# Performance work log

Measured on AMD Instinct MI355X. Metric: run time of the kernel, lower is better.

Reference implementation:

```python
import jax, jax.numpy as jnp
import numpy as np

DIM = 1024
DIM_HEAD = 64
HEADS = 8
INNER = DIM_HEAD * HEADS
EPS = 1e-5


def layernorm(x, g, b):
    mu = jnp.mean(x, axis=-1, keepdims=True)
    var = jnp.var(x, axis=-1, keepdims=True)
    return (x - mu) * jax.lax.rsqrt(var + EPS) * g + b


def setup_inputs() -> dict:
    key = jax.random.key(0)
    ks = jax.random.split(key, 8)
    b, n, m = 8, 4096, 64
    x = jax.random.normal(ks[0], (b, n, DIM), dtype=jnp.float32)
    latents = jax.random.normal(ks[1], (b, m, DIM), dtype=jnp.float32)
    mask = jax.random.bernoulli(ks[2], 0.9, (b, n))
    s = DIM ** -0.5
    Wq = jax.random.normal(ks[3], (DIM, INNER), dtype=jnp.float32) * s
    Wkv = jax.random.normal(ks[4], (DIM, 2 * INNER), dtype=jnp.float32) * s
    Wo = jax.random.normal(ks[5], (INNER, DIM), dtype=jnp.float32) * (INNER ** -0.5)
    ln_x_g = jnp.ones((DIM,), jnp.float32); ln_x_b = jnp.zeros((DIM,), jnp.float32)
    ln_l_g = jnp.ones((DIM,), jnp.float32); ln_l_b = jnp.zeros((DIM,), jnp.float32)
    ln_o_g = jnp.ones((DIM,), jnp.float32); ln_o_b = jnp.zeros((DIM,), jnp.float32)
    return {"x": x, "latents": latents, "mask": mask,
            "Wq": Wq, "Wkv": Wkv, "Wo": Wo,
            "ln_x_g": ln_x_g, "ln_x_b": ln_x_b,
            "ln_l_g": ln_l_g, "ln_l_b": ln_l_b,
            "ln_o_g": ln_o_g, "ln_o_b": ln_o_b}


def reference(x, latents, mask, Wq, Wkv, Wo, ln_x_g, ln_x_b, ln_l_g, ln_l_b, ln_o_g, ln_o_b):
    scale = DIM_HEAD ** -0.5
    b, m = latents.shape[0], latents.shape[1]
    xn = layernorm(x, ln_x_g, ln_x_b)
    ln = layernorm(latents, ln_l_g, ln_l_b)
    q = ln @ Wq                                   # [b, m, inner]
    kv_in = jnp.concatenate([xn, ln], axis=1)     # [b, n+m, dim]
    kv = kv_in @ Wkv                              # [b, n+m, 2*inner]
    k, v = jnp.split(kv, 2, axis=-1)
    # b n (h d) -> b h n d
    q = q.reshape(b, m, HEADS, DIM_HEAD).transpose(0, 2, 1, 3)
    k = k.reshape(b, k.shape[1], HEADS, DIM_HEAD).transpose(0, 2, 1, 3)
    v = v.reshape(b, v.shape[1], HEADS, DIM_HEAD).transpose(0, 2, 1, 3)
    # NOTE: scale applied twice, faithful to the original module.
    sim = jnp.einsum('bhid,bhjd->bhij', q * scale, k) * scale
    full_mask = jnp.concatenate([mask, jnp.ones((b, m), dtype=bool)], axis=1)  # pad True for latents
    max_neg = -jnp.finfo(sim.dtype).max
    sim = jnp.where(full_mask[:, None, None, :], sim, max_neg)
    attn = jax.nn.softmax(sim.astype(jnp.float32), axis=-1).astype(sim.dtype)
    out = jnp.einsum('bhij,bhjd->bhid', attn, v)
    out = out.transpose(0, 2, 1, 3).reshape(b, m, INNER)
    out = out @ Wo
    return layernorm(out, ln_o_g, ln_o_b)
```

## Files before the change

kernel.cpp:

```cpp
#include <hip/hip_runtime.h>

typedef unsigned short u16;
typedef unsigned int u32;
using f32x4  = __attribute__((ext_vector_type(4))) float;
using short8 = __attribute__((ext_vector_type(8))) short;
using s16x4  = __attribute__((ext_vector_type(4))) short;
using u16x4  = __attribute__((ext_vector_type(4))) unsigned short;

#define DEV __device__ __forceinline__

DEV u16 f2bf(float f) {
  u32 u = __float_as_uint(f);
  u32 r = u + 0x7fffu + ((u >> 16) & 1u);
  return (u16)(r >> 16);
}

DEV void gload_lds16(const void* g, void* l) {
  __builtin_amdgcn_global_load_lds(
      (__attribute__((address_space(1))) void*)g,
      (__attribute__((address_space(3))) void*)l, 16, 0, 0);
}

DEV void block_reduce2(float& a, float& b, float* red) {
#pragma unroll
  for (int m = 1; m < 64; m <<= 1) {
    a += __shfl_xor(a, m);
    b += __shfl_xor(b, m);
  }
  const int wid = threadIdx.x >> 6, lane = threadIdx.x & 63;
  __syncthreads();
  if (lane == 0) { red[wid] = a; red[4 + wid] = b; }
  __syncthreads();
  a = red[0] + red[1] + red[2] + red[3];
  b = red[4] + red[5] + red[6] + red[7];
}

__global__ __launch_bounds__(256) void ln_rows_k(
    const float* __restrict__ X, const float* __restrict__ g,
    const float* __restrict__ be, u16* __restrict__ out, int mode)
{
  __shared__ float red[8];
  const int r = blockIdx.x, t = threadIdx.x;
  const float4 v = *(const float4*)(X + (((size_t)r) << 10) + t * 4);
  float s1 = v.x + v.y + v.z + v.w;
  float s2 = v.x * v.x + v.y * v.y + v.z * v.z + v.w * v.w;
  block_reduce2(s1, s2, red);
  const float mean = s1 * (1.f / 1024.f);
  const float var  = s2 * (1.f / 1024.f) - mean * mean;
  const float rstd = rsqrtf(var + 1e-5f);
  const float4 gv = *(const float4*)(g + t * 4);
  const float4 bv = *(const float4*)(be + t * 4);
  u16x4 o;
  o[0] = f2bf((v.x - mean) * rstd * gv.x + bv.x);
  o[1] = f2bf((v.y - mean) * rstd * gv.y + bv.y);
  o[2] = f2bf((v.z - mean) * rstd * gv.z + bv.z);
  o[3] = f2bf((v.w - mean) * rstd * gv.w + bv.w);
  const size_t orow = (mode == 0)
      ? ((size_t)(r >> 12) * 4160 + (r & 4095))
      : ((size_t)(r >> 6) * 4160 + 4096 + (r & 63));
  *(u16x4*)(out + orow * 1024 + t * 4) = o;
}

__global__ __launch_bounds__(256) void transpose_w_k(
    const float* __restrict__ W, u16* __restrict__ Wt, int K, int N)
{
  __shared__ float tile[32][33];
  const int n0 = blockIdx.x * 32, k0 = blockIdx.y * 32;
  const int tx = threadIdx.x, ty = threadIdx.y;
#pragma unroll
  for (int i = 0; i < 4; ++i)
    tile[ty + 8 * i][tx] = W[(size_t)(k0 + ty + 8 * i) * N + n0 + tx];
  __syncthreads();
#pragma unroll
  for (int i = 0; i < 4; ++i)
    Wt[(size_t)(n0 + ty + 8 * i) * K + k0 + tx] = f2bf(tile[tx][ty + 8 * i]);
}

__global__ __launch_bounds__(256) void mask_bias_k(const void* __restrict__ mask,
                                                   float* __restrict__ bias)
{
  __shared__ int flag_s;
  if (threadIdx.x == 0) {
    const u32* mw = (const u32*)mask;
    bool fpat = true, ipat = true;
    for (int i = 0; i < 256; ++i) {
      u32 w = mw[i];
      if (w != 0u && w != 0x3f800000u) fpat = false;
      if (w > 1u) ipat = false;
    }
    flag_s = fpat ? 2 : (ipat ? 1 : 0);
  }
  __syncthreads();
  const int flag = flag_s;
  const int idx = blockIdx.x * 256 + threadIdx.x;
  const int b = idx / 4160, j = idx - b * 4160;
  float bv = 0.f;
  if (j < 4096) {
    const int mi = b * 4096 + j;
    bool on;
    if (flag == 2)      on = ((const float*)mask)[mi] != 0.f;
    else if (flag == 1) on = ((const int*)mask)[mi] != 0;
    else                on = ((const unsigned char*)mask)[mi] != 0;
    bv = on ? 0.f : -1e30f;
  }
  bias[idx] = bv;
}

template <int MODE>
__global__ __launch_bounds__(256) void gemm_k(
    const u16* __restrict__ A, const u16* __restrict__ Bt, u16* __restrict__ out)
{
  __shared__ __attribute__((aligned(16))) short As[4096];
  __shared__ __attribute__((aligned(16))) short Bs[4096];
  const int tid = threadIdx.x;
  const int wid = tid >> 6, lane = tid & 63;
  const int wm = wid >> 1, wn = wid & 1;
  const int m0 = blockIdx.x * 128, n0 = blockIdx.y * 128;
  const f32x4 z4 = {0.f, 0.f, 0.f, 0.f};
  f32x4 acc[4][4];
#pragma unroll
  for (int i = 0; i < 4; ++i)
#pragma unroll
    for (int j = 0; j < 4; ++j) acc[i][j] = z4;

  for (int kt = 0; kt < 32; ++kt) {
    const int k0 = kt * 32;
#pragma unroll
    for (int p = 0; p < 2; ++p) {
      const int idx = p * 256 + tid;
      const int row = idx >> 2, seg = idx & 3;
      size_t ar;
      if (MODE == 1) {
        const int gr = m0 + row;
        ar = (size_t)(gr >> 6) * 4160 + 4096 + (gr & 63);
      } else {
        ar = (size_t)(m0 + row);
      }
      gload_lds16(A + ar * 1024 + k0 + seg * 8, &As[(p * 256 + wid * 64) * 8]);
    }
#pragma unroll
    for (int p = 0; p < 2; ++p) {
      const int idx = p * 256 + tid;
      const int row = idx >> 2, seg = idx & 3;
      gload_lds16(Bt + (size_t)(n0 + row) * 1024 + k0 + seg * 8,
                  &Bs[(p * 256 + wid * 64) * 8]);
    }
    __syncthreads();
    short8 af[4], bfr[4];
#pragma unroll
    for (int mi = 0; mi < 4; ++mi)
      af[mi] = *(const short8*)&As[(wm * 64 + mi * 16 + (lane & 15)) * 32 + 8 * (lane >> 4)];
#pragma unroll
    for (int ni = 0; ni < 4; ++ni)
      bfr[ni] = *(const short8*)&Bs[(wn * 64 + ni * 16 + (lane & 15)) * 32 + 8 * (lane >> 4)];
#pragma unroll
    for (int mi = 0; mi < 4; ++mi)
#pragma unroll
      for (int ni = 0; ni < 4; ++ni)
        acc[mi][ni] = __builtin_amdgcn_mfma_f32_16x16x32_bf16(af[mi], bfr[ni], acc[mi][ni], 0, 0, 0);
    __syncthreads();
  }

#pragma unroll
  for (int mi = 0; mi < 4; ++mi)
#pragma unroll
    for (int ni = 0; ni < 4; ++ni)
#pragma unroll
      for (int r = 0; r < 4; ++r) {
        const int gm = m0 + wm * 64 + mi * 16 + (lane >> 4) * 4 + r;
        const int gn = n0 + wn * 64 + ni * 16 + (lane & 15);
        const u16 v = f2bf(acc[mi][ni][r]);
        if (MODE == 0) {
          const int b = gm / 4160, j = gm - b * 4160;
          out[(((size_t)b * 8 + (gn >> 6)) * 4160 + j) * 64 + (gn & 63)] = v;
        } else if (MODE == 1) {
          const int b = gm >> 6, i = gm & 63;
          out[(((size_t)b * 8 + (gn >> 6)) * 64 + i) * 64 + (gn & 63)] = v;
        } else {
          const int b = gn / 4160, j = gn - b * 4160;
          out[(((size_t)b * 8 + (gm >> 6)) * 64 + (gm & 63)) * 4160 + j] = v;
        }
      }
}

__global__ __launch_bounds__(256) void attn_k(
    const u16* __restrict__ q_h, const u16* __restrict__ k_h,
    const u16* __restrict__ v_t, const float* __restrict__ bias,
    float* __restrict__ O_part, float* __restrict__ m_part,
    float* __restrict__ l_part)
{
  __shared__ __attribute__((aligned(16))) short Ks[4096];
  __shared__ __attribute__((aligned(16))) short Vs[4096];
  __shared__ __attribute__((aligned(16))) short Ps[4][1152];
  __shared__ float biasS[64];
  const int bid = blockIdx.x;
  const int sp = bid & 7, bh = bid >> 3;
  const int b = bh >> 3;
  const int tid = threadIdx.x, wid = tid >> 6, lane = tid & 63;
  const int t0 = sp ? (8 * sp + 1) : 0;
  const int tc = sp ? 8 : 9;

  const size_t qoff = ((size_t)bh * 64 + wid * 16 + (lane & 15)) * 64 + 8 * (lane >> 4);
  const short8 qf0 = *(const short8*)&q_h[qoff];
  const short8 qf1 = *(const short8*)&q_h[qoff + 32];

  float mrun = -1e30f, lrun = 0.f;
  const f32x4 z4 = {0.f, 0.f, 0.f, 0.f};
  f32x4 o[4] = {z4, z4, z4, z4};
  const size_t khead = (size_t)bh * (4160 * 64);
  const size_t vhead = (size_t)bh * (64 * 4160);

  for (int tt = 0; tt < tc; ++tt) {
    const int t = t0 + tt;
#pragma unroll
    for (int p = 0; p < 2; ++p) {
      const int lo = (p * 256 + tid) * 16;
      const int row = lo >> 7;
      const int src = lo ^ ((row & 7) << 4);
      gload_lds16((const char*)k_h + (khead + (size_t)t * 4096) * 2 + src,
                  (char*)Ks + (p * 256 + wid * 64) * 16);
    }
#pragma unroll
    for (int p = 0; p < 2; ++p) {
      const int lo = (p * 256 + tid) * 16;
      const int row = lo >> 7;
      const int colb = (lo ^ ((row & 7) << 4)) & 127;
      gload_lds16((const char*)v_t + (vhead + (size_t)row * 4160 + t * 64) * 2 + colb,
                  (char*)Vs + (p * 256 + wid * 64) * 16);
    }
    if (tid < 64) biasS[tid] = bias[b * 4160 + t * 64 + tid];
    __syncthreads();

    f32x4 sc[4] = {z4, z4, z4, z4};
#pragma unroll
    for (int mi = 0; mi < 4; ++mi) {
      const int row = mi * 16 + (lane & 15);
      const int sw = (row & 7) << 4;
      short8 a0 = *(const short8*)((const char*)Ks + ((row * 128 + 16 * (lane >> 4)) ^ sw));
      sc[mi] = __builtin_amdgcn_mfma_f32_16x16x32_bf16(a0, qf0, sc[mi], 0, 0, 0);
      short8 a1 = *(const short8*)((const char*)Ks + ((row * 128 + 64 + 16 * (lane >> 4)) ^ sw));
      sc[mi] = __builtin_amdgcn_mfma_f32_16x16x32_bf16(a1, qf1, sc[mi], 0, 0, 0);
    }

    float sv[4][4];
    float tmax = -3e30f;
#pragma unroll
    for (int mi = 0; mi < 4; ++mi)
#pragma unroll
      for (int r = 0; r < 4; ++r) {
        const int kv = mi * 16 + (lane >> 4) * 4 + r;
        const float s = sc[mi][r] * (1.f / 64.f) + biasS[kv];
        sv[mi][r] = s;
        tmax = fmaxf(tmax, s);
      }
    tmax = fmaxf(tmax, __shfl_xor(tmax, 16));
    tmax = fmaxf(tmax, __shfl_xor(tmax, 32));
    const float mnew = fmaxf(mrun, tmax);
    const float fac = __expf(mrun - mnew);
    float psum = 0.f;
#pragma unroll
    for (int mi = 0; mi < 4; ++mi) {
      s16x4 pk;
#pragma unroll
      for (int r = 0; r < 4; ++r) {
        const float p = __expf(sv[mi][r] - mnew);
        psum += p;
        pk[r] = (short)f2bf(p);
      }
      *(s16x4*)&Ps[wid][(lane & 15) * 72 + mi * 16 + (lane >> 4) * 4] = pk;
    }
    psum += __shfl_xor(psum, 16);
    psum += __shfl_xor(psum, 32);
    lrun = lrun * fac + psum;
    mrun = mnew;
#pragma unroll
    for (int mi = 0; mi < 4; ++mi)
#pragma unroll
      for (int e = 0; e < 4; ++e) o[mi][e] *= fac;

#pragma unroll
    for (int mi = 0; mi < 4; ++mi) {
      const int row = mi * 16 + (lane & 15);
      const int sw = (row & 7) << 4;
      short8 a0 = *(const short8*)((const char*)Vs + ((row * 128 + 16 * (lane >> 4)) ^ sw));
      short8 p0 = *(const short8*)&Ps[wid][(lane & 15) * 72 + 8 * (lane >> 4)];
      o[mi] = __builtin_amdgcn_mfma_f32_16x16x32_bf16(a0, p0, o[mi], 0, 0, 0);
      short8 a1 = *(const short8*)((const char*)Vs + ((row * 128 + 64 + 16 * (lane >> 4)) ^ sw));
      short8 p1 = *(const short8*)&Ps[wid][(lane & 15) * 72 + 32 + 8 * (lane >> 4)];
      o[mi] = __builtin_amdgcn_mfma_f32_16x16x32_bf16(a1, p1, o[mi], 0, 0, 0);
    }
    __syncthreads();
  }

#pragma unroll
  for (int mi = 0; mi < 4; ++mi)
#pragma unroll
    for (int r = 0; r < 4; ++r) {
      const int d = mi * 16 + (lane >> 4) * 4 + r;
      const int q = wid * 16 + (lane & 15);
      O_part[(((size_t)sp * 64 + bh) * 64 + d) * 64 + q] = o[mi][r];
    }
  if (lane < 16) {
    m_part[((size_t)sp * 64 + bh) * 64 + wid * 16 + lane] = mrun;
    l_part[((size_t)sp * 64 + bh) * 64 + wid * 16 + lane] = lrun;
  }
}

__global__ __launch_bounds__(256) void combine_k(
    const float* __restrict__ O_part, const float* __restrict__ m_part,
    const float* __restrict__ l_part, float* __restrict__ attn_out)
{
  __shared__ float wgt[8][64];
  const int bh = blockIdx.x;
  const int b = bh >> 3, h = bh & 7;
  const int t = threadIdx.x;
  if (t < 64) {
    float mv[8], lv[8];
#pragma unroll
    for (int s = 0; s < 8; ++s) {
      mv[s] = m_part[((size_t)s * 64 + bh) * 64 + t];
      lv[s] = l_part[((size_t)s * 64 + bh) * 64 + t];
    }
    float M = mv[0];
#pragma unroll
    for (int s = 1; s < 8; ++s) M = fmaxf(M, mv[s]);
    float den = 0.f;
#pragma unroll
    for (int s = 0; s < 8; ++s) den += lv[s] * __expf(mv[s] - M);
    const float inv = 1.f / den;
#pragma unroll
    for (int s = 0; s < 8; ++s) wgt[s][t] = __expf(mv[s] - M) * inv;
  }
  __syncthreads();
#pragma unroll
  for (int i = 0; i < 16; ++i) {
    const int p = i * 256 + t;
    const int d = p >> 6, q = p & 63;
    float acc = 0.f;
#pragma unroll
    for (int s = 0; s < 8; ++s)
      acc += O_part[(((size_t)s * 64 + bh) * 64 + d) * 64 + q] * wgt[s][q];
    attn_out[((size_t)b * 64 + q) * 512 + h * 64 + d] = acc;
  }
}

__global__ __launch_bounds__(256) void outproj_k(
    const float* __restrict__ attn_out, const float* __restrict__ Wo,
    const float* __restrict__ g, const float* __restrict__ be,
    float* __restrict__ out)
{
  __shared__ float arow[2][512];
  __shared__ float red[8];
  const int rb = blockIdx.x * 2, t = threadIdx.x;
  arow[0][t]       = attn_out[(size_t)rb * 512 + t];
  arow[0][t + 256] = attn_out[(size_t)rb * 512 + 256 + t];
  arow[1][t]       = attn_out[(size_t)(rb + 1) * 512 + t];
  arow[1][t + 256] = attn_out[(size_t)(rb + 1) * 512 + 256 + t];
  __syncthreads();
  float a0x = 0, a0y = 0, a0z = 0, a0w = 0;
  float a1x = 0, a1y = 0, a1z = 0, a1w = 0;
  for (int k = 0; k < 512; ++k) {
    const float4 w = *(const float4*)(Wo + (size_t)k * 1024 + t * 4);
    const float x0 = arow[0][k], x1 = arow[1][k];
    a0x += x0 * w.x; a0y += x0 * w.y; a0z += x0 * w.z; a0w += x0 * w.w;
    a1x += x1 * w.x; a1y += x1 * w.y; a1z += x1 * w.z; a1w += x1 * w.w;
  }
  const float4 gv = *(const float4*)(g + t * 4);
  const float4 bv = *(const float4*)(be + t * 4);
  {
    float s1 = a0x + a0y + a0z + a0w;
    float s2 = a0x * a0x + a0y * a0y + a0z * a0z + a0w * a0w;
    block_reduce2(s1, s2, red);
    const float mean = s1 * (1.f / 1024.f);
    const float rstd = rsqrtf(s2 * (1.f / 1024.f) - mean * mean + 1e-5f);
    float4 ov;
    ov.x = (a0x - mean) * rstd * gv.x + bv.x;
    ov.y = (a0y - mean) * rstd * gv.y + bv.y;
    ov.z = (a0z - mean) * rstd * gv.z + bv.z;
    ov.w = (a0w - mean) * rstd * gv.w + bv.w;
    *(float4*)(out + (size_t)rb * 1024 + t * 4) = ov;
  }
  {
    float s1 = a1x + a1y + a1z + a1w;
    float s2 = a1x * a1x + a1y * a1y + a1z * a1z + a1w * a1w;
    block_reduce2(s1, s2, red);
    const float mean = s1 * (1.f / 1024.f);
    const float rstd = rsqrtf(s2 * (1.f / 1024.f) - mean * mean + 1e-5f);
    float4 ov;
    ov.x = (a1x - mean) * rstd * gv.x + bv.x;
    ov.y = (a1y - mean) * rstd * gv.y + bv.y;
    ov.z = (a1z - mean) * rstd * gv.z + bv.z;
    ov.w = (a1w - mean) * rstd * gv.w + bv.w;
    *(float4*)(out + (size_t)(rb + 1) * 1024 + t * 4) = ov;
  }
}

extern "C" void kernel_launch(void* const* d_in, const int* in_sizes, int n_in,
                              void* d_out, int out_size, void* d_ws, size_t ws_size,
                              hipStream_t stream) {
  (void)in_sizes; (void)n_in; (void)out_size; (void)ws_size;
  const float* x       = (const float*)d_in[0];
  const float* latents = (const float*)d_in[1];
  const void*  mask    = d_in[2];
  const float* Wq      = (const float*)d_in[3];
  const float* Wkv     = (const float*)d_in[4];
  const float* Wo      = (const float*)d_in[5];
  const float* gx      = (const float*)d_in[6];
  const float* bx      = (const float*)d_in[7];
  const float* gl      = (const float*)d_in[8];
  const float* bl      = (const float*)d_in[9];
  const float* go      = (const float*)d_in[10];
  const float* bo      = (const float*)d_in[11];
  float* out = (float*)d_out;

  char* w = (char*)d_ws;
  u16* xnl   = (u16*)w; w += (size_t)33280 * 1024 * 2;
  u16* Wq_t  = (u16*)w; w += (size_t)512 * 1024 * 2;
  u16* Wkv_t = (u16*)w; w += (size_t)1024 * 1024 * 2;
  u16* q_h   = (u16*)w; w += (size_t)8 * 8 * 64 * 64 * 2;
  u16* k_h   = (u16*)w; w += (size_t)8 * 8 * 4160 * 64 * 2;
  u16* v_t   = (u16*)w; w += (size_t)8 * 8 * 64 * 4160 * 2;
  float* bias   = (float*)w; w += (size_t)8 * 4160 * 4;
  float* O_part = (float*)w; w += (size_t)8 * 64 * 64 * 64 * 4;
  float* m_part = (float*)w; w += (size_t)8 * 64 * 64 * 4;
  float* l_part = (float*)w; w += (size_t)8 * 64 * 64 * 4;
  float* attnO  = (float*)w; w += (size_t)512 * 512 * 4;

  transpose_w_k<<<dim3(16, 32), dim3(32, 8), 0, stream>>>(Wq, Wq_t, 1024, 512);
  transpose_w_k<<<dim3(32, 32), dim3(32, 8), 0, stream>>>(Wkv, Wkv_t, 1024, 1024);
  ln_rows_k<<<dim3(32768), dim3(256), 0, stream>>>(x, gx, bx, xnl, 0);
  ln_rows_k<<<dim3(512), dim3(256), 0, stream>>>(latents, gl, bl, xnl, 1);
  mask_bias_k<<<dim3(130), dim3(256), 0, stream>>>(mask, bias);
  gemm_k<1><<<dim3(4, 4), dim3(256), 0, stream>>>(xnl, Wq_t, q_h);
  gemm_k<0><<<dim3(260, 4), dim3(256), 0, stream>>>(xnl, Wkv_t, k_h);
  gemm_k<2><<<dim3(4, 260), dim3(256), 0, stream>>>(Wkv_t + (size_t)512 * 1024, xnl, v_t);
  attn_k<<<dim3(512), dim3(256), 0, stream>>>(q_h, k_h, v_t, bias, O_part, m_part, l_part);
  combine_k<<<dim3(64), dim3(256), 0, stream>>>(O_part, m_part, l_part, attnO);
  outproj_k<<<dim3(256), dim3(256), 0, stream>>>(attnO, Wo, go, bo, out);
}
```

Baseline: 262.2 us.

## Fuse Q/K/V projections into one pipelined 256x256-tile GEMM kernel

Replaces three separate 128x128-tile GEMM launches with one kernel that dispatches Q, K and V^T tiles by block index. It uses 256x256 tiles with 8 waves and double-buffered LDS filled by global_load_lds. Stage loads are interleaved between MFMA phases, with XOR-swizzled LDS rows and s_setprio around the MFMA bursts. The aim is more operand reuse, hidden load latency, fewer LDS bank conflicts and fewer launches. In exchange it uses a large LDS footprint that limits occupancy, and 524 big blocks may leave an uneven tail across CUs.

After: 248.3 us. 1.06x faster.

```diff
diff --git a/kernel.cpp b/kernel.cpp
--- a/kernel.cpp
+++ b/kernel.cpp
@@ -106,81 +106,181 @@
   bias[idx] = bv;
 }
 
-template <int MODE>
-__global__ __launch_bounds__(256) void gemm_k(
-    const u16* __restrict__ A, const u16* __restrict__ Bt, u16* __restrict__ out)
-{
-  __shared__ __attribute__((aligned(16))) short As[4096];
-  __shared__ __attribute__((aligned(16))) short Bs[4096];
-  const int tid = threadIdx.x;
-  const int wid = tid >> 6, lane = tid & 63;
-  const int wm = wid >> 1, wn = wid & 1;
-  const int m0 = blockIdx.x * 128, n0 = blockIdx.y * 128;
+__global__ __launch_bounds__(512, 2) void gemm8_k(
+    const u16* __restrict__ xnl, const u16* __restrict__ Wq_t,
+    const u16* __restrict__ Wkv_t,
+    u16* __restrict__ q_h, u16* __restrict__ k_h, u16* __restrict__ v_t)
+{
+  __shared__ __attribute__((aligned(16))) short As[2][16384];
+  __shared__ __attribute__((aligned(16))) short Bs[2][16384];
+
+  const int tid = threadIdx.x, wid = tid >> 6, lane = tid & 63;
+  const int wr = wid >> 2, wc = wid & 3;
+  const int l15 = lane & 15, lq = lane >> 4;
+
+  const int bid = blockIdx.x;
+  int mode, mblk, nblk;
+  const u16 *Ap, *Bp;
+  if (bid < 260)      { mode = 0; mblk = bid % 130; nblk = bid / 130; Ap = xnl; Bp = Wkv_t; }
+  else if (bid < 520) { const int r2 = bid - 260; mode = 2; mblk = r2 / 130; nblk = r2 % 130;
+                        Ap = Wkv_t + (size_t)512 * 1024; Bp = xnl; }
+  else                { const int r2 = bid - 520; mode = 1; mblk = r2 >> 1; nblk = r2 & 1;
+                        Ap = xnl; Bp = Wq_t; }
+  const int m0 = mblk * 256, n0 = nblk * 256;
+  const bool remap = (mode == 1);
+
+  auto stageA = [&](int c, int T, int half, int i) {
+    const int g = half * 1024 + i * 512 + tid;
+    const int row = g >> 3, slot = g & 7;
+    const int gr = m0 + row;
+    const size_t ar = remap ? ((size_t)(gr >> 6) * 4160 + 4096 + (gr & 63)) : (size_t)gr;
+    gload_lds16(Ap + ar * 1024 + T * 64 + ((slot ^ (row & 7)) * 8),
+                &As[c][(half * 1024 + i * 512 + wid * 64) * 8]);
+  };
+  auto stageB = [&](int c, int T, int half, int i) {
+    const int g = half * 1024 + i * 512 + tid;
+    const int row = g >> 3, slot = g & 7;
+    gload_lds16(Bp + (size_t)(n0 + row) * 1024 + T * 64 + ((slot ^ (row & 7)) * 8),
+                &Bs[c][(half * 1024 + i * 512 + wid * 64) * 8]);
+  };
+  auto readA = [&](int c, int r, int w) -> short8 {
+    const int inner = (w * 64 + lq * 16) ^ ((r & 7) << 4);
+    return *(const short8*)((const char*)&As[c][0] + r * 128 + inner);
+  };
+  auto readB = [&](int c, int r, int w) -> short8 {
+    const int inner = (w * 64 + lq * 16) ^ ((r & 7) << 4);
+    return *(const short8*)((const char*)&Bs[c][0] + r * 128 + inner);
+  };
+
   const f32x4 z4 = {0.f, 0.f, 0.f, 0.f};
-  f32x4 acc[4][4];
-#pragma unroll
-  for (int i = 0; i < 4; ++i)
+  f32x4 acc[8][4];
+#pragma unroll
+  for (int i = 0; i < 8; ++i)
 #pragma unroll
     for (int j = 0; j < 4; ++j) acc[i][j] = z4;
 
-  for (int kt = 0; kt < 32; ++kt) {
-    const int k0 = kt * 32;
-#pragma unroll
-    for (int p = 0; p < 2; ++p) {
-      const int idx = p * 256 + tid;
-      const int row = idx >> 2, seg = idx & 3;
-      size_t ar;
-      if (MODE == 1) {
-        const int gr = m0 + row;
-        ar = (size_t)(gr >> 6) * 4160 + 4096 + (gr & 63);
-      } else {
-        ar = (size_t)(m0 + row);
-      }
-      gload_lds16(A + ar * 1024 + k0 + seg * 8, &As[(p * 256 + wid * 64) * 8]);
-    }
-#pragma unroll
-    for (int p = 0; p < 2; ++p) {
-      const int idx = p * 256 + tid;
-      const int row = idx >> 2, seg = idx & 3;
-      gload_lds16(Bt + (size_t)(n0 + row) * 1024 + k0 + seg * 8,
-                  &Bs[(p * 256 + wid * 64) * 8]);
-    }
-    __syncthreads();
-    short8 af[4], bfr[4];
-#pragma unroll
-    for (int mi = 0; mi < 4; ++mi)
-      af[mi] = *(const short8*)&As[(wm * 64 + mi * 16 + (lane & 15)) * 32 + 8 * (lane >> 4)];
-#pragma unroll
-    for (int ni = 0; ni < 4; ++ni)
-      bfr[ni] = *(const short8*)&Bs[(wn * 64 + ni * 16 + (lane & 15)) * 32 + 8 * (lane >> 4)];
-#pragma unroll
-    for (int mi = 0; mi < 4; ++mi)
-#pragma unroll
-      for (int ni = 0; ni < 4; ++ni)
-        acc[mi][ni] = __builtin_amdgcn_mfma_f32_16x16x32_bf16(af[mi], bfr[ni], acc[mi][ni], 0, 0, 0);
-    __syncthreads();
-  }
-
-#pragma unroll
-  for (int mi = 0; mi < 4; ++mi)
-#pragma unroll
-    for (int ni = 0; ni < 4; ++ni)
+#pragma unroll
+  for (int T = 0; T < 2; ++T) {
+    stageA(T, T, 0, 0); stageA(T, T, 0, 1);
+    stageB(T, T, 0, 0); stageB(T, T, 0, 1);
+    stageB(T, T, 1, 0); stageB(T, T, 1, 1);
+    stageA(T, T, 1, 0); stageA(T, T, 1, 1);
+  }
+
+  short8 af[4][2], bf0[2][2], bf1[2][2];
+
+#pragma unroll 1
+  for (int t = 0; t < 16; ++t) {
+    const int c = t & 1;
+    if (t == 15) { asm volatile("s_waitcnt vmcnt(0)" ::: "memory"); }
+    else         { asm volatile("s_waitcnt vmcnt(8)" ::: "memory"); }
+    __builtin_amdgcn_s_barrier();
+
+#pragma unroll
+    for (int mi = 0; mi < 4; ++mi)
+#pragma unroll
+      for (int w = 0; w < 2; ++w)
+        af[mi][w] = readA(c, wr * 64 + mi * 16 + l15, w);
+#pragma unroll
+    for (int nj = 0; nj < 2; ++nj)
+#pragma unroll
+      for (int w = 0; w < 2; ++w)
+        bf0[nj][w] = readB(c, wc * 32 + nj * 16 + l15, w);
+    __builtin_amdgcn_s_barrier();
+    asm volatile("s_waitcnt lgkmcnt(0)" ::: "memory");
+    __builtin_amdgcn_sched_barrier(0);
+    __builtin_amdgcn_s_setprio(1);
+#pragma unroll
+    for (int mi = 0; mi < 4; ++mi)
+#pragma unroll
+      for (int nj = 0; nj < 2; ++nj)
+#pragma unroll
+        for (int w = 0; w < 2; ++w)
+          acc[mi][nj] = __builtin_amdgcn_mfma_f32_16x16x32_bf16(af[mi][w], bf0[nj][w], acc[mi][nj], 0, 0, 0);
+    __builtin_amdgcn_s_setprio(0);
+    __builtin_amdgcn_s_barrier();
+
+#pragma unroll
+    for (int nj = 0; nj < 2; ++nj)
+#pragma unroll
+      for (int w = 0; w < 2; ++w)
+        bf1[nj][w] = readB(c, 128 + wc * 32 + nj * 16 + l15, w);
+    if (t < 14) {
+      stageA(c, t + 2, 0, 0); stageA(c, t + 2, 0, 1);
+      stageB(c, t + 2, 0, 0); stageB(c, t + 2, 0, 1);
+    }
+    __builtin_amdgcn_s_barrier();
+    asm volatile("s_waitcnt lgkmcnt(0)" ::: "memory");
+    __builtin_amdgcn_sched_barrier(0);
+    __builtin_amdgcn_s_setprio(1);
+#pragma unroll
+    for (int mi = 0; mi < 4; ++mi)
+#pragma unroll
+      for (int nj = 0; nj < 2; ++nj)
+#pragma unroll
+        for (int w = 0; w < 2; ++w)
+          acc[mi][2 + nj] = __builtin_amdgcn_mfma_f32_16x16x32_bf16(af[mi][w], bf1[nj][w], acc[mi][2 + nj], 0, 0, 0);
+    __builtin_amdgcn_s_setprio(0);
+    __builtin_amdgcn_s_barrier();
+
+#pragma unroll
+    for (int mi = 0; mi < 4; ++mi)
+#pragma unroll
+      for (int w = 0; w < 2; ++w)
+        af[mi][w] = readA(c, 128 + wr * 64 + mi * 16 + l15, w);
+    if (t < 14) { stageB(c, t + 2, 1, 0); stageB(c, t + 2, 1, 1); }
+    __builtin_amdgcn_s_barrier();
+    asm volatile("s_waitcnt lgkmcnt(0)" ::: "memory");
+    __builtin_amdgcn_sched_barrier(0);
+    __builtin_amdgcn_s_setprio(1);
+#pragma unroll
+    for (int mi = 0; mi < 4; ++mi)
+#pragma unroll
+      for (int nj = 0; nj < 2; ++nj)
+#pragma unroll
+        for (int w = 0; w < 2; ++w)
+          acc[4 + mi][nj] = __builtin_amdgcn_mfma_f32_16x16x32_bf16(af[mi][w], bf0[nj][w], acc[4 + mi][nj], 0, 0, 0);
+    __builtin_amdgcn_s_setprio(0);
+    __builtin_amdgcn_s_barrier();
+
+    if (t < 14) { stageA(c, t + 2, 1, 0); stageA(c, t + 2, 1, 1); }
+    __builtin_amdgcn_s_barrier();
+    __builtin_amdgcn_s_setprio(1);
+#pragma unroll
+    for (int mi = 0; mi < 4; ++mi)
+#pragma unroll
+      for (int nj = 0; nj < 2; ++nj)
+#pragma unroll
+        for (int w = 0; w < 2; ++w)
+          acc[4 + mi][2 + nj] = __builtin_amdgcn_mfma_f32_16x16x32_bf16(af[mi][w], bf1[nj][w], acc[4 + mi][2 + nj], 0, 0, 0);
+    __builtin_amdgcn_s_setprio(0);
+    __builtin_amdgcn_s_barrier();
+  }
+
+#pragma unroll
+  for (int ai = 0; ai < 8; ++ai) {
+    const int mh = ai >> 2, mi = ai & 3;
+#pragma unroll
+    for (int bi = 0; bi < 4; ++bi) {
+      const int nh = bi >> 1, nj = bi & 1;
+      const int gn = n0 + nh * 128 + wc * 32 + nj * 16 + l15;
 #pragma unroll
       for (int r = 0; r < 4; ++r) {
-        const int gm = m0 + wm * 64 + mi * 16 + (lane >> 4) * 4 + r;
-        const int gn = n0 + wn * 64 + ni * 16 + (lane & 15);
-        const u16 v = f2bf(acc[mi][ni][r]);
-        if (MODE == 0) {
+        const int gm = m0 + mh * 128 + wr * 64 + mi * 16 + lq * 4 + r;
+        const u16 v = f2bf(acc[ai][bi][r]);
+        if (mode == 0) {
           const int b = gm / 4160, j = gm - b * 4160;
-          out[(((size_t)b * 8 + (gn >> 6)) * 4160 + j) * 64 + (gn & 63)] = v;
-        } else if (MODE == 1) {
-          const int b = gm >> 6, i = gm & 63;
-          out[(((size_t)b * 8 + (gn >> 6)) * 64 + i) * 64 + (gn & 63)] = v;
+          k_h[(((size_t)b * 8 + (gn >> 6)) * 4160 + j) * 64 + (gn & 63)] = v;
+        } else if (mode == 2) {
+          const int b = gn / 4160, j = gn - b * 4160;
+          v_t[(((size_t)b * 8 + (gm >> 6)) * 64 + (gm & 63)) * 4160 + j] = v;
         } else {
-          const int b = gn / 4160, j = gn - b * 4160;
-          out[(((size_t)b * 8 + (gm >> 6)) * 64 + (gm & 63)) * 4160 + j] = v;
+          const int b = gm >> 6, i2 = gm & 63;
+          q_h[(((size_t)b * 8 + (gn >> 6)) * 64 + i2) * 64 + (gn & 63)] = v;
         }
       }
+    }
+  }
 }
 
 __global__ __launch_bounds__(256) void attn_k(
@@ -431,9 +531,7 @@
   ln_rows_k<<<dim3(32768), dim3(256), 0, stream>>>(x, gx, bx, xnl, 0);
   ln_rows_k<<<dim3(512), dim3(256), 0, stream>>>(latents, gl, bl, xnl, 1);
   mask_bias_k<<<dim3(130), dim3(256), 0, stream>>>(mask, bias);
-  gemm_k<1><<<dim3(4, 4), dim3(256), 0, stream>>>(xnl, Wq_t, q_h);
-  gemm_k<0><<<dim3(260, 4), dim3(256), 0, stream>>>(xnl, Wkv_t, k_h);
-  gemm_k<2><<<dim3(4, 260), dim3(256), 0, stream>>>(Wkv_t + (size_t)512 * 1024, xnl, v_t);
+  gemm8_k<<<dim3(524), dim3(512), 0, stream>>>(xnl, Wq_t, Wkv_t, q_h, k_h, v_t);
   attn_k<<<dim3(512), dim3(256), 0, stream>>>(q_h, k_h, v_t, bias, O_part, m_part, l_part);
   combine_k<<<dim3(64), dim3(256), 0, stream>>>(O_part, m_part, l_part, attnO);
   outproj_k<<<dim3(256), dim3(256), 0, stream>>>(attnO, Wo, go, bo, out);
```

## Merge projection GEMMs into one triple-buffered swizzled 128x256 tile kernel

Applied to the files above, without the earlier changes.

Replaces three separate GEMM launches (Q, K, V-transposed) with a single kernel that dispatches on block index. Each block now computes a 128x256 tile with 8 waves. It uses a 3-stage LDS ring with async global-to-LDS loads, partial vmcnt waits and a single barrier per k-step. LDS is XOR-swizzled to avoid bank conflicts, and MFMA sections get raised wave priority. This is meant to overlap loads with compute, remove per-launch overhead and tail effects, and raise MFMA utilisation, at the cost of more LDS per block and possibly lower occupancy.

New measurement: 245.1 us. 1.07x faster.

```diff
diff --git a/kernel.cpp b/kernel.cpp
--- a/kernel.cpp
+++ b/kernel.cpp
@@ -106,16 +106,40 @@
   bias[idx] = bv;
 }
 
-template <int MODE>
-__global__ __launch_bounds__(256) void gemm_k(
-    const u16* __restrict__ A, const u16* __restrict__ Bt, u16* __restrict__ out)
-{
-  __shared__ __attribute__((aligned(16))) short As[4096];
-  __shared__ __attribute__((aligned(16))) short Bs[4096];
-  const int tid = threadIdx.x;
-  const int wid = tid >> 6, lane = tid & 63;
-  const int wm = wid >> 1, wn = wid & 1;
-  const int m0 = blockIdx.x * 128, n0 = blockIdx.y * 128;
+__global__ __launch_bounds__(512, 4) void gemm2_k(
+    const u16* __restrict__ xnl, const u16* __restrict__ Wq_t,
+    const u16* __restrict__ Wkv_t,
+    u16* __restrict__ q_h, u16* __restrict__ k_h, u16* __restrict__ v_t)
+{
+  __shared__ __attribute__((aligned(16))) short As[3][4096];
+  __shared__ __attribute__((aligned(16))) short Bs[3][8192];
+
+  const int tid = threadIdx.x, lane = tid & 63;
+  const int wid = tid >> 6, wr = wid >> 2, wc = wid & 3;
+  const int l15 = lane & 15, lq = lane >> 4;
+
+  const int bid = blockIdx.x;
+  int mode, mblk, nblk;
+  const u16 *Ap, *Bp;
+  if (bid < 520)       { mode = 0; mblk = bid % 260; nblk = bid / 260; Ap = xnl; Bp = Wkv_t; }
+  else if (bid < 1040) { const int r2 = bid - 520; mode = 2; mblk = r2 & 3; nblk = r2 >> 2;
+                         Ap = Wkv_t + (size_t)512 * 1024; Bp = xnl; }
+  else                 { const int r2 = bid - 1040; mode = 1; mblk = r2 >> 1; nblk = r2 & 1;
+                         Ap = xnl; Bp = Wq_t; }
+  const int m0 = mblk * 128, n0 = nblk * 256;
+
+  const int srow = tid >> 2, sslot = tid & 3;
+  const u32 ss = (u32)((sslot ^ ((srow >> 1) & 3)) * 8);
+  const int gra = m0 + srow;
+  const u32 arow = (mode == 1) ? ((u32)(gra >> 6) * 4160u + 4096u + (u32)(gra & 63)) : (u32)gra;
+  const u32 aoff  = arow * 1024u + ss;
+  const u32 boff0 = (u32)(n0 + srow) * 1024u + ss;
+  const u32 boff1 = (u32)(n0 + 128 + srow) * 1024u + ss;
+
+  const int rsw = ((lq ^ ((l15 >> 1) & 3)) << 4);
+  const int aRd = wr * 4096 + l15 * 64 + rsw;
+  const int bRd = wc * 4096 + l15 * 64 + rsw;
+
   const f32x4 z4 = {0.f, 0.f, 0.f, 0.f};
   f32x4 acc[4][4];
 #pragma unroll
@@ -123,62 +147,59 @@
 #pragma unroll
     for (int j = 0; j < 4; ++j) acc[i][j] = z4;
 
-  for (int kt = 0; kt < 32; ++kt) {
-    const int k0 = kt * 32;
-#pragma unroll
-    for (int p = 0; p < 2; ++p) {
-      const int idx = p * 256 + tid;
-      const int row = idx >> 2, seg = idx & 3;
-      size_t ar;
-      if (MODE == 1) {
-        const int gr = m0 + row;
-        ar = (size_t)(gr >> 6) * 4160 + 4096 + (gr & 63);
-      } else {
-        ar = (size_t)(m0 + row);
-      }
-      gload_lds16(A + ar * 1024 + k0 + seg * 8, &As[(p * 256 + wid * 64) * 8]);
-    }
-#pragma unroll
-    for (int p = 0; p < 2; ++p) {
-      const int idx = p * 256 + tid;
-      const int row = idx >> 2, seg = idx & 3;
-      gload_lds16(Bt + (size_t)(n0 + row) * 1024 + k0 + seg * 8,
-                  &Bs[(p * 256 + wid * 64) * 8]);
-    }
-    __syncthreads();
-    short8 af[4], bfr[4];
+  auto stage = [&](int buf, int T) {
+    gload_lds16(Ap + aoff  + (u32)T * 32u, &As[buf][tid * 8]);
+    gload_lds16(Bp + boff0 + (u32)T * 32u, &Bs[buf][tid * 8]);
+    gload_lds16(Bp + boff1 + (u32)T * 32u, &Bs[buf][4096 + tid * 8]);
+  };
+
+  stage(0, 0);
+  stage(1, 1);
+  asm volatile("s_waitcnt vmcnt(3)" ::: "memory");
+  __builtin_amdgcn_s_barrier();
+
+  int c0 = 0, c1 = 1, c2 = 2;
+#pragma unroll 1
+  for (int t = 0; t < 32; ++t) {
+    if (t < 30) stage(c2, t + 2);
+    const char* aB = (const char*)&As[0][0] + c0 * 8192  + aRd;
+    const char* bB = (const char*)&Bs[0][0] + c0 * 16384 + bRd;
+    short8 af[4], bf[4];
+#pragma unroll
+    for (int mi = 0; mi < 4; ++mi) af[mi] = *(const short8*)(aB + mi * 1024);
+#pragma unroll
+    for (int nj = 0; nj < 4; ++nj) bf[nj] = *(const short8*)(bB + nj * 1024);
+    __builtin_amdgcn_s_setprio(1);
 #pragma unroll
     for (int mi = 0; mi < 4; ++mi)
-      af[mi] = *(const short8*)&As[(wm * 64 + mi * 16 + (lane & 15)) * 32 + 8 * (lane >> 4)];
-#pragma unroll
-    for (int ni = 0; ni < 4; ++ni)
-      bfr[ni] = *(const short8*)&Bs[(wn * 64 + ni * 16 + (lane & 15)) * 32 + 8 * (lane >> 4)];
-#pragma unroll
-    for (int mi = 0; mi < 4; ++mi)
-#pragma unroll
-      for (int ni = 0; ni < 4; ++ni)
-        acc[mi][ni] = __builtin_amdgcn_mfma_f32_16x16x32_bf16(af[mi], bfr[ni], acc[mi][ni], 0, 0, 0);
-    __syncthreads();
+#pragma unroll
+      for (int nj = 0; nj < 4; ++nj)
+        acc[mi][nj] = __builtin_amdgcn_mfma_f32_16x16x32_bf16(af[mi], bf[nj], acc[mi][nj], 0, 0, 0);
+    __builtin_amdgcn_s_setprio(0);
+    if (t < 30)       { asm volatile("s_waitcnt vmcnt(3)" ::: "memory"); }
+    else if (t == 30) { asm volatile("s_waitcnt vmcnt(0)" ::: "memory"); }
+    __builtin_amdgcn_s_barrier();
+    const int tmp = c0; c0 = c1; c1 = c2; c2 = tmp;
   }
 
 #pragma unroll
   for (int mi = 0; mi < 4; ++mi)
 #pragma unroll
-    for (int ni = 0; ni < 4; ++ni)
+    for (int nj = 0; nj < 4; ++nj)
 #pragma unroll
       for (int r = 0; r < 4; ++r) {
-        const int gm = m0 + wm * 64 + mi * 16 + (lane >> 4) * 4 + r;
-        const int gn = n0 + wn * 64 + ni * 16 + (lane & 15);
-        const u16 v = f2bf(acc[mi][ni][r]);
-        if (MODE == 0) {
+        const int gm = m0 + wr * 64 + mi * 16 + lq * 4 + r;
+        const int gn = n0 + wc * 64 + nj * 16 + l15;
+        const u16 v = f2bf(acc[mi][nj][r]);
+        if (mode == 0) {
           const int b = gm / 4160, j = gm - b * 4160;
-          out[(((size_t)b * 8 + (gn >> 6)) * 4160 + j) * 64 + (gn & 63)] = v;
-        } else if (MODE == 1) {
-          const int b = gm >> 6, i = gm & 63;
-          out[(((size_t)b * 8 + (gn >> 6)) * 64 + i) * 64 + (gn & 63)] = v;
+          k_h[(((size_t)b * 8 + (gn >> 6)) * 4160 + j) * 64 + (gn & 63)] = v;
+        } else if (mode == 2) {
+          const int b = gn / 4160, j = gn - b * 4160;
+          v_t[(((size_t)b * 8 + (gm >> 6)) * 64 + (gm & 63)) * 4160 + j] = v;
         } else {
-          const int b = gn / 4160, j = gn - b * 4160;
-          out[(((size_t)b * 8 + (gm >> 6)) * 64 + (gm & 63)) * 4160 + j] = v;
+          const int b = gm >> 6, i2 = gm & 63;
+          q_h[(((size_t)b * 8 + (gn >> 6)) * 64 + i2) * 64 + (gn & 63)] = v;
         }
       }
 }
@@ -431,9 +452,7 @@
   ln_rows_k<<<dim3(32768), dim3(256), 0, stream>>>(x, gx, bx, xnl, 0);
   ln_rows_k<<<dim3(512), dim3(256), 0, stream>>>(latents, gl, bl, xnl, 1);
   mask_bias_k<<<dim3(130), dim3(256), 0, stream>>>(mask, bias);
-  gemm_k<1><<<dim3(4, 4), dim3(256), 0, stream>>>(xnl, Wq_t, q_h);
-  gemm_k<0><<<dim3(260, 4), dim3(256), 0, stream>>>(xnl, Wkv_t, k_h);
-  gemm_k<2><<<dim3(4, 260), dim3(256), 0, stream>>>(Wkv_t + (size_t)512 * 1024, xnl, v_t);
+  gemm2_k<<<dim3(1048), dim3(512), 0, stream>>>(xnl, Wq_t, Wkv_t, q_h, k_h, v_t);
   attn_k<<<dim3(512), dim3(256), 0, stream>>>(q_h, k_h, v_t, bias, O_part, m_part, l_part);
   combine_k<<<dim3(64), dim3(256), 0, stream>>>(O_part, m_part, l_part, attnO);
   outproj_k<<<dim3(256), dim3(256), 0, stream>>>(attnO, Wo, go, bo, out);
```
